# Kernel tuning notes

Measured on AMD Instinct MI355X. Metric: run time of the kernel, lower is better.

The kernel has to match this reference:

```python
import jax, jax.numpy as jnp
import numpy as np

LAMBDA = 0.2
BETA = 1.0
EPS = 1e-6


def setup_inputs() -> dict:
    key = jax.random.key(0)
    t_prime = jax.random.normal(key, (8192, 768), dtype=jnp.float32)
    return {"t_prime": t_prime}


def reference(t_prime) -> jnp.ndarray:
    vocab = t_prime.shape[0]
    # L2-normalize rows (matches F.normalize p=2, dim=1 with its 1e-12 clamp)
    norm = jnp.maximum(jnp.linalg.norm(t_prime, axis=1, keepdims=True), 1e-12)
    t_norm = t_prime / norm
    # [vocab, vocab] cosine similarity
    S = t_norm @ t_norm.T
    diag = jnp.diagonal(S)
    collapse = jnp.sum((diag - 1.0) ** 2)
    # HNS path: off-diagonal entries per row, expressed without boolean reshape.
    # neg_sims = S with diagonal removed; reweight * neg^2 = beta * neg^3 / (mean_neg + eps)
    S_off = S - jnp.diag(diag)  # zero diagonal == off-diagonal values
    mean_neg = jnp.sum(S_off, axis=1) / (vocab - 1)  # per-row mean of negatives
    row_cube = jnp.sum(S_off ** 3, axis=1)  # diagonal contributes 0
    hard_neg_loss = BETA * jnp.sum(row_cube / (mean_neg + EPS))
    return collapse + LAMBDA * hard_neg_loss
```

## Files before the change

kernel.cpp:

```cpp
#include <hip/hip_runtime.h>
#include <math.h>

#define VV 8192
#define DD 768
#define NDMAX 256

typedef __attribute__((ext_vector_type(8))) short bf16x8;
typedef __attribute__((ext_vector_type(4))) float f32x4;

__device__ inline ushort f2bf(float f) {
    uint u = __float_as_uint(f);
    uint r = (u + 0x7fffu + ((u >> 16) & 1u)) >> 16;
    return (ushort)r;
}
__device__ inline float bf2f(ushort h) { return __uint_as_float(((uint)h) << 16); }

__device__ inline void gload16(const ushort* g, ushort* l) {
    __builtin_amdgcn_global_load_lds(
        (const __attribute__((address_space(1))) void*)g,
        (__attribute__((address_space(3))) void*)l, 16, 0, 0);
}

__global__ __launch_bounds__(256) void k_normfused(const float* __restrict__ t,
                                                   float* __restrict__ norms,
                                                   ushort* __restrict__ xh,
                                                   ushort* __restrict__ xl,
                                                   double* __restrict__ gp,
                                                   float* __restrict__ rc,
                                                   int* __restrict__ dlist,
                                                   int* __restrict__ dcount) {
    const int tid = threadIdx.x;
    const int r0 = blockIdx.x * 16;
    if (tid < 16) rc[r0 + tid] = 0.f;
    if (blockIdx.x == 0) {
        dlist[tid] = -1;
        if (tid == 0) *dcount = 0;
    }
    __shared__ double wsum[2][4];
    const int lane = tid & 63, w = tid >> 6;
    double s0 = 0.0, s1 = 0.0, s2 = 0.0;
    for (int rr = 0; rr < 16; rr += 2) {
        const float* trA = t + (size_t)(r0 + rr) * DD;
        const float* trB = trA + DD;
        float a0 = trA[tid], a1 = trA[tid + 256], a2 = trA[tid + 512];
        float b0 = trB[tid], b1 = trB[tid + 256], b2 = trB[tid + 512];
        double sA = (double)a0 * a0 + (double)a1 * a1 + (double)a2 * a2;
        double sB = (double)b0 * b0 + (double)b1 * b1 + (double)b2 * b2;
#pragma unroll
        for (int o = 32; o > 0; o >>= 1) {
            sA += __shfl_down(sA, o, 64);
            sB += __shfl_down(sB, o, 64);
        }
        if (lane == 0) { wsum[0][w] = sA; wsum[1][w] = sB; }
        __syncthreads();
        float nA = fmaxf((float)sqrt(wsum[0][0] + wsum[0][1] + wsum[0][2] + wsum[0][3]), 1e-12f);
        float nB = fmaxf((float)sqrt(wsum[1][0] + wsum[1][1] + wsum[1][2] + wsum[1][3]), 1e-12f);
        __syncthreads();
        if (tid == 0) {
            norms[r0 + rr] = nA;
            norms[r0 + rr + 1] = nB;
        }
        size_t baseA = (size_t)(r0 + rr) * DD, baseB = baseA + DD;
        float xA0 = a0 / nA, xA1 = a1 / nA, xA2 = a2 / nA;
        float xB0 = b0 / nB, xB1 = b1 / nB, xB2 = b2 / nB;
        ushort h;
        h = f2bf(xA0); xh[baseA + tid] = h;       xl[baseA + tid] = f2bf(xA0 - bf2f(h));
        h = f2bf(xA1); xh[baseA + tid + 256] = h; xl[baseA + tid + 256] = f2bf(xA1 - bf2f(h));
        h = f2bf(xA2); xh[baseA + tid + 512] = h; xl[baseA + tid + 512] = f2bf(xA2 - bf2f(h));
        h = f2bf(xB0); xh[baseB + tid] = h;       xl[baseB + tid] = f2bf(xB0 - bf2f(h));
        h = f2bf(xB1); xh[baseB + tid + 256] = h; xl[baseB + tid + 256] = f2bf(xB1 - bf2f(h));
        h = f2bf(xB2); xh[baseB + tid + 512] = h; xl[baseB + tid + 512] = f2bf(xB2 - bf2f(h));
        s0 += (double)xA0; s0 += (double)xB0;
        s1 += (double)xA1; s1 += (double)xB1;
        s2 += (double)xA2; s2 += (double)xB2;
    }
    double* gb = gp + (size_t)blockIdx.x * DD;
    gb[tid] = s0;
    gb[tid + 256] = s1;
    gb[tid + 512] = s2;
}

__global__ __launch_bounds__(256) void k_colsumB(const double* __restrict__ gp,
                                                 double* __restrict__ g) {
    __shared__ double red[8][32];
    int c = threadIdx.x & 31, part = threadIdx.x >> 5;
    int col = blockIdx.x * 32 + c;
    double s = 0.0;
    for (int b = part * 64; b < part * 64 + 64; ++b)
        s += gp[(size_t)b * DD + col];
    red[part][c] = s;
    __syncthreads();
    if (part == 0) {
        double tt = 0.0;
        for (int p = 0; p < 8; ++p) tt += red[p][c];
        g[col] = tt;
    }
}

__global__ __launch_bounds__(256) void k_mean(const float* __restrict__ t,
                                              const float* __restrict__ norms,
                                              const double* __restrict__ g,
                                              double* __restrict__ mnum,
                                              double* __restrict__ dd,
                                              int* __restrict__ dlist,
                                              int* __restrict__ dcount) {
    int r = blockIdx.x * 4 + (threadIdx.x >> 6);
    int lane = threadIdx.x & 63;
    const float* tr = t + (size_t)r * DD;
    float nrm = norms[r];
    double xg = 0.0, xx = 0.0;
#pragma unroll
    for (int k = lane; k < DD; k += 64) {
        float xf = tr[k] / nrm;
        double xv = (double)xf;
        xg += xv * g[k];
        xx += xv * xv;
    }
#pragma unroll
    for (int o = 32; o > 0; o >>= 1) {
        xg += __shfl_down(xg, o, 64);
        xx += __shfl_down(xx, o, 64);
    }
    if (lane == 0) {
        double m = xg - xx;
        mnum[r] = m;
        dd[r] = xx;
        if (fabs(m / 8191.0 + 1e-6) < 1e-5) {
            int pos = atomicAdd(dcount, 1);
            if (pos < NDMAX) dlist[pos] = r;
        }
    }
}

__global__ __launch_bounds__(256, 2) void k_cube(const ushort* __restrict__ xh,
                                                 const ushort* __restrict__ xl,
                                                 const int* __restrict__ dlist,
                                                 float* __restrict__ Sb,
                                                 float* __restrict__ rc) {
    __shared__ ushort As0[4096], As1[4096], As2[4096];
    __shared__ ushort Bs0[8192], Bs1[8192], Bs2[8192];

    const int bid = blockIdx.x;
    const int tid = threadIdx.x;
    const int lane = tid & 63;
    const int wid = tid >> 6;
    const int l15 = lane & 15, li4 = lane >> 4;
    const int wm = wid >> 1, wn = wid & 1;

    const bool strip = (bid < 192);
    int bi = 0, bj = 0, seg = 0, rp = 0, cp = 0;
    if (strip) {
        seg = bid >> 6;
        int rem = bid & 63;
        rp = rem >> 5;
        cp = rem & 31;
        if (dlist[rp * 128] < 0) return;
    } else {
        int idx = bid - 192;
        int wg = (idx & 7) * 132 + (idx >> 3);
        int j = 0;
        while (wg >= 2 * j + 2) { wg -= 2 * j + 2; ++j; }
        bi = wg;
        bj = j;
    }
    const ushort* XA = strip ? ((seg == 1) ? xl : xh) : xh;
    const ushort* XB = strip ? ((seg == 2) ? xl : xh) : xh;

    int asrc[2], bsrc[4], lda_[2], ldb_[4];
#pragma unroll
    for (int j = 0; j < 2; ++j) {
        int li = tid + j * 256;
        int row = li >> 2;
        int sl = ((li & 3) ^ ((li >> 3) & 3)) * 8;
        int ar = strip ? dlist[rp * 128 + row] : (bi * 128 + row);
        if (ar < 0) ar = 0;
        asrc[j] = ar * DD + sl;
        lda_[j] = li * 8;
    }
#pragma unroll
    for (int j = 0; j < 4; ++j) {
        int li = tid + j * 256;
        int row = li >> 2;
        int sl = ((li & 3) ^ ((li >> 3) & 3)) * 8;
        int br = strip ? (cp * 256 + row) : (bj * 256 + row);
        bsrc[j] = br * DD + sl;
        ldb_[j] = li * 8;
    }

    const int swz = (li4 ^ ((l15 >> 1) & 3)) << 3;
    const int aoff = (wm * 64 + l15) * 32 + swz;
    const int boff = (wn * 128 + l15) * 32 + swz;

    f32x4 acc[4][8];
#pragma unroll
    for (int f = 0; f < 4; ++f)
#pragma unroll
        for (int n = 0; n < 8; ++n) acc[f][n] = (f32x4){0.f, 0.f, 0.f, 0.f};

#define STG(AW, BW, KT)                                  \
    do {                                                 \
        const int kq_ = (KT) * 32;                       \
        gload16(XA + asrc[0] + kq_, (AW) + lda_[0]);     \
        gload16(XA + asrc[1] + kq_, (AW) + lda_[1]);     \
        gload16(XB + bsrc[0] + kq_, (BW) + ldb_[0]);     \
        gload16(XB + bsrc[1] + kq_, (BW) + ldb_[1]);     \
        gload16(XB + bsrc[2] + kq_, (BW) + ldb_[2]);     \
        gload16(XB + bsrc[3] + kq_, (BW) + ldb_[3]);     \
    } while (0)

#define COMPUTE(AR, BR)                                                     \
    do {                                                                    \
        bf16x8 av[4], bv[8];                                                \
        _Pragma("unroll") for (int f = 0; f < 4; ++f)                       \
            av[f] = *(const bf16x8*)((AR) + aoff + f * 512);                \
        _Pragma("unroll") for (int n = 0; n < 8; ++n)                       \
            bv[n] = *(const bf16x8*)((BR) + boff + n * 512);                \
        _Pragma("unroll") for (int f = 0; f < 4; ++f)                       \
            _Pragma("unroll") for (int n = 0; n < 8; ++n)                   \
                acc[f][n] = __builtin_amdgcn_mfma_f32_16x16x32_bf16(        \
                    av[f], bv[n], acc[f][n], 0, 0, 0);                      \
    } while (0)

#define VMW6() asm volatile("s_waitcnt vmcnt(6)" ::: "memory")
#define VMW0() asm volatile("s_waitcnt vmcnt(0)" ::: "memory")
#define RBAR() asm volatile("s_barrier" ::: "memory")

    STG(As0, Bs0, 0);
    STG(As1, Bs1, 1);
    VMW6(); RBAR();

    for (int tb = 0; tb < 21; tb += 3) {
        STG(As2, Bs2, tb + 2);
        COMPUTE(As0, Bs0);
        VMW6(); RBAR();
        STG(As0, Bs0, tb + 3);
        COMPUTE(As1, Bs1);
        VMW6(); RBAR();
        STG(As1, Bs1, tb + 4);
        COMPUTE(As2, Bs2);
        VMW6(); RBAR();
    }
    STG(As2, Bs2, 23);
    COMPUTE(As0, Bs0);
    VMW6(); RBAR();
    COMPUTE(As1, Bs1);
    VMW0(); RBAR();
    COMPUTE(As2, Bs2);
#undef STG
#undef COMPUTE
#undef VMW6
#undef VMW0
#undef RBAR

    if (strip) {
#pragma unroll
        for (int f = 0; f < 4; ++f)
#pragma unroll
            for (int n = 0; n < 8; ++n)
#pragma unroll
                for (int r = 0; r < 4; ++r) {
                    int slot = seg * 256 + rp * 128 + wm * 64 + f * 16 + li4 * 4 + r;
                    int col = cp * 256 + wn * 128 + n * 16 + l15;
                    Sb[((size_t)slot << 13) + col] = acc[f][n][r];
                }
        return;
    }

    const bool dtile = ((bi >> 1) == bj);
    const int R0 = bi * 128, C0 = bj * 256;
    float rsum[4][4], csum[8];
#pragma unroll
    for (int n = 0; n < 8; ++n) csum[n] = 0.f;
#pragma unroll
    for (int f = 0; f < 4; ++f)
#pragma unroll
        for (int r = 0; r < 4; ++r) rsum[f][r] = 0.f;
#pragma unroll
    for (int f = 0; f < 4; ++f)
#pragma unroll
        for (int n = 0; n < 8; ++n)
#pragma unroll
            for (int r = 0; r < 4; ++r) {
                float s = acc[f][n][r];
                float c = s * s * s;
                int ri = R0 + wm * 64 + f * 16 + li4 * 4 + r;
                int cj = C0 + wn * 128 + n * 16 + l15;
                if (dtile && ri == cj) c = 0.f;
                rsum[f][r] += c;
                csum[n] += c;
            }
#pragma unroll
    for (int o = 1; o < 16; o <<= 1)
#pragma unroll
        for (int f = 0; f < 4; ++f)
#pragma unroll
            for (int r = 0; r < 4; ++r)
                rsum[f][r] += __shfl_xor(rsum[f][r], o, 64);
    if (l15 == 0) {
#pragma unroll
        for (int f = 0; f < 4; ++f)
#pragma unroll
            for (int r = 0; r < 4; ++r)
                atomicAdd(&rc[R0 + wm * 64 + f * 16 + li4 * 4 + r], rsum[f][r]);
    }
    if (!dtile) {
#pragma unroll
        for (int o = 16; o < 64; o <<= 1)
#pragma unroll
            for (int n = 0; n < 8; ++n) csum[n] += __shfl_xor(csum[n], o, 64);
        if (li4 == 0) {
#pragma unroll
            for (int n = 0; n < 8; ++n)
                atomicAdd(&rc[C0 + wn * 128 + n * 16 + l15], csum[n]);
        }
    }
}

__global__ __launch_bounds__(256) void k_cubefin(const float* __restrict__ Sb,
                                                 const int* __restrict__ dlist,
                                                 float* __restrict__ rc) {
    const int slot = blockIdx.x;
    const int drow = dlist[slot];
    if (drow < 0) return;
    const int tid = threadIdx.x;
    const float* s0p = Sb + ((size_t)slot << 13);
    const float* s1p = Sb + ((size_t)(256 + slot) << 13);
    const float* s2p = Sb + ((size_t)(512 + slot) << 13);
    float sum = 0.f;
    for (int c = tid; c < VV; c += 256) {
        float s0 = s0p[c];
        float sf = s0 + s1p[c] + s2p[c];
        float d = sf * sf * sf - s0 * s0 * s0;
        if (c == drow) d = 0.f;
        sum += d;
    }
    __shared__ float red[256];
    red[tid] = sum;
    __syncthreads();
    for (int o = 128; o > 0; o >>= 1) {
        if (tid < o) red[tid] += red[tid + o];
        __syncthreads();
    }
    if (tid == 0) atomicAdd(&rc[drow], red[0]);
}

__global__ __launch_bounds__(1024) void k_final(const float* __restrict__ rc,
                                                const double* __restrict__ mnum,
                                                const double* __restrict__ dd,
                                                float* __restrict__ out) {
    int tid = threadIdx.x;
    double acc = 0.0, col = 0.0;
    for (int r = tid; r < VV; r += 1024) {
        double m = mnum[r] / 8191.0 + 1e-6;
        acc += (double)rc[r] / m;
        double dm = dd[r] - 1.0;
        col += dm * dm;
    }
    __shared__ double sa[1024], sc[1024];
    sa[tid] = acc;
    sc[tid] = col;
    __syncthreads();
    for (int o = 512; o > 0; o >>= 1) {
        if (tid < o) {
            sa[tid] += sa[tid + o];
            sc[tid] += sc[tid + o];
        }
        __syncthreads();
    }
    if (tid == 0) out[0] = (float)(sc[0] + 0.2 * sa[0]);
}

extern "C" void kernel_launch(void* const* d_in, const int* in_sizes, int n_in,
                              void* d_out, int out_size, void* d_ws, size_t ws_size,
                              hipStream_t stream) {
    const float* t = (const float*)d_in[0];
    float* out = (float*)d_out;

    char* ws = (char*)d_ws;
    float* Sb = (float*)ws;
    size_t off = (size_t)VV * DD * sizeof(float);
    ushort* xh = (ushort*)(ws + off); off += (size_t)VV * DD * sizeof(ushort);
    ushort* xl = (ushort*)(ws + off); off += (size_t)VV * DD * sizeof(ushort);
    double* g = (double*)(ws + off);  off += DD * sizeof(double);
    double* mnum = (double*)(ws + off); off += VV * sizeof(double);
    double* dd = (double*)(ws + off);  off += VV * sizeof(double);
    float* rc = (float*)(ws + off);    off += VV * sizeof(float);
    int* dlist = (int*)(ws + off);     off += NDMAX * sizeof(int);
    int* dcount = (int*)(ws + off);    off += sizeof(int) + 60;
    float* norms = (float*)(ws + off); off += VV * sizeof(float);
    double* gp = (double*)(ws + off);  off += (size_t)512 * DD * sizeof(double);

    k_normfused<<<512, 256, 0, stream>>>(t, norms, xh, xl, gp, rc, dlist, dcount);
    k_colsumB<<<24, 256, 0, stream>>>(gp, g);
    k_mean<<<VV / 4, 256, 0, stream>>>(t, norms, g, mnum, dd, dlist, dcount);
    k_cube<<<1248, 256, 0, stream>>>(xh, xl, dlist, Sb, rc);
    k_cubefin<<<NDMAX, 256, 0, stream>>>(Sb, dlist, rc);
    k_final<<<1, 1024, 0, stream>>>(rc, mnum, dd, out);
}
```

Before: 121.1 us.

## Split tail triangle tiles into half-width blocks to balance final wave

The last 224 triangle tiles of the symmetric S=XX^T cube-sum kernel are now each split into two 128x128 half tiles, handled by extra blocks (1472 instead of 1248). The main loop moves into a templated helper so half blocks load and multiply only half the B columns, with their own epilogue for row and column cube sums. The aim is to shrink the tail wave imbalance across CUs. The cost is extra A-tile reloads and more atomics for those tiles.

```diff
diff --git a/kernel.cpp b/kernel.cpp
--- a/kernel.cpp
+++ b/kernel.cpp
@@ -132,6 +132,81 @@
     }
 }
 
+template <int NLB>
+__device__ __forceinline__ void cube_loop(
+    const ushort* __restrict__ XA, const ushort* __restrict__ XB,
+    int asrc0, int asrc1, int bsrc0, int bsrc1, int bsrc2, int bsrc3,
+    int lda0, int lda1, int ldb0, int ldb1, int ldb2, int ldb3,
+    int aoff, int boff,
+    ushort* As0, ushort* As1, ushort* As2,
+    ushort* Bs0, ushort* Bs1, ushort* Bs2,
+    f32x4 (&acc)[4][8]) {
+    constexpr int NB = 2 * NLB;
+
+#define STG(AW, BW, KT)                                                  \
+    do {                                                                 \
+        const int kq_ = (KT) * 32;                                       \
+        gload16(XA + asrc0 + kq_, (AW) + lda0);                          \
+        gload16(XA + asrc1 + kq_, (AW) + lda1);                          \
+        gload16(XB + bsrc0 + kq_, (BW) + ldb0);                          \
+        gload16(XB + bsrc1 + kq_, (BW) + ldb1);                          \
+        if constexpr (NLB == 4) {                                        \
+            gload16(XB + bsrc2 + kq_, (BW) + ldb2);                      \
+            gload16(XB + bsrc3 + kq_, (BW) + ldb3);                      \
+        }                                                                \
+    } while (0)
+
+#define COMPUTE(AR, BR)                                                     \
+    do {                                                                    \
+        bf16x8 av[4], bv[NB];                                               \
+        _Pragma("unroll") for (int f = 0; f < 4; ++f)                       \
+            av[f] = *(const bf16x8*)((AR) + aoff + f * 512);                \
+        _Pragma("unroll") for (int n = 0; n < NB; ++n)                      \
+            bv[n] = *(const bf16x8*)((BR) + boff + n * 512);                \
+        _Pragma("unroll") for (int f = 0; f < 4; ++f)                       \
+            _Pragma("unroll") for (int n = 0; n < NB; ++n)                  \
+                acc[f][n] = __builtin_amdgcn_mfma_f32_16x16x32_bf16(        \
+                    av[f], bv[n], acc[f][n], 0, 0, 0);                      \
+    } while (0)
+
+#define VMWP()                                                           \
+    do {                                                                 \
+        if constexpr (NLB == 4)                                          \
+            asm volatile("s_waitcnt vmcnt(6)" ::: "memory");              \
+        else                                                             \
+            asm volatile("s_waitcnt vmcnt(4)" ::: "memory");              \
+    } while (0)
+#define VMW0() asm volatile("s_waitcnt vmcnt(0)" ::: "memory")
+#define RBAR() asm volatile("s_barrier" ::: "memory")
+
+    STG(As0, Bs0, 0);
+    STG(As1, Bs1, 1);
+    VMWP(); RBAR();
+
+    for (int tb = 0; tb < 21; tb += 3) {
+        STG(As2, Bs2, tb + 2);
+        COMPUTE(As0, Bs0);
+        VMWP(); RBAR();
+        STG(As0, Bs0, tb + 3);
+        COMPUTE(As1, Bs1);
+        VMWP(); RBAR();
+        STG(As1, Bs1, tb + 4);
+        COMPUTE(As2, Bs2);
+        VMWP(); RBAR();
+    }
+    STG(As2, Bs2, 23);
+    COMPUTE(As0, Bs0);
+    VMWP(); RBAR();
+    COMPUTE(As1, Bs1);
+    VMW0(); RBAR();
+    COMPUTE(As2, Bs2);
+#undef STG
+#undef COMPUTE
+#undef VMWP
+#undef VMW0
+#undef RBAR
+}
+
 __global__ __launch_bounds__(256, 2) void k_cube(const ushort* __restrict__ xh,
                                                  const ushort* __restrict__ xl,
                                                  const int* __restrict__ dlist,
@@ -148,7 +223,8 @@
     const int wm = wid >> 1, wn = wid & 1;
 
     const bool strip = (bid < 192);
-    int bi = 0, bj = 0, seg = 0, rp = 0, cp = 0;
+    const bool half = (bid >= 1024);
+    int bi = 0, bj = 0, seg = 0, rp = 0, cp = 0, hh = 0;
     if (strip) {
         seg = bid >> 6;
         int rem = bid & 63;
@@ -156,8 +232,16 @@
         cp = rem & 31;
         if (dlist[rp * 128] < 0) return;
     } else {
-        int idx = bid - 192;
-        int wg = (idx & 7) * 132 + (idx >> 3);
+        int wg;
+        if (!half) {
+            int idx = bid - 192;
+            wg = (idx & 7) * 132 + (idx >> 3);
+        } else {
+            int hx = bid - 1024;
+            int q = hx >> 1;
+            hh = hx & 1;
+            wg = (q & 7) * 132 + 104 + (q >> 3);
+        }
         int j = 0;
         while (wg >= 2 * j + 2) { wg -= 2 * j + 2; ++j; }
         bi = wg;
@@ -166,7 +250,7 @@
     const ushort* XA = strip ? ((seg == 1) ? xl : xh) : xh;
     const ushort* XB = strip ? ((seg == 2) ? xl : xh) : xh;
 
-    int asrc[2], bsrc[4], lda_[2], ldb_[4];
+    int asrc[2], bsrc[4] = {0, 0, 0, 0}, lda_[2], ldb_[4] = {0, 0, 0, 0};
 #pragma unroll
     for (int j = 0; j < 2; ++j) {
         int li = tid + j * 256;
@@ -177,19 +261,20 @@
         asrc[j] = ar * DD + sl;
         lda_[j] = li * 8;
     }
-#pragma unroll
-    for (int j = 0; j < 4; ++j) {
+    const int nbl = half ? 2 : 4;
+    for (int j = 0; j < nbl; ++j) {
         int li = tid + j * 256;
         int row = li >> 2;
         int sl = ((li & 3) ^ ((li >> 3) & 3)) * 8;
-        int br = strip ? (cp * 256 + row) : (bj * 256 + row);
+        int br = strip ? (cp * 256 + row)
+                       : (bj * 256 + (half ? hh * 128 : 0) + row);
         bsrc[j] = br * DD + sl;
         ldb_[j] = li * 8;
     }
 
     const int swz = (li4 ^ ((l15 >> 1) & 3)) << 3;
     const int aoff = (wm * 64 + l15) * 32 + swz;
-    const int boff = (wn * 128 + l15) * 32 + swz;
+    const int boff = ((wn * (half ? 64 : 128)) + l15) * 32 + swz;
 
     f32x4 acc[4][8];
 #pragma unroll
@@ -197,60 +282,64 @@
 #pragma unroll
         for (int n = 0; n < 8; ++n) acc[f][n] = (f32x4){0.f, 0.f, 0.f, 0.f};
 
-#define STG(AW, BW, KT)                                  \
-    do {                                                 \
-        const int kq_ = (KT) * 32;                       \
-        gload16(XA + asrc[0] + kq_, (AW) + lda_[0]);     \
-        gload16(XA + asrc[1] + kq_, (AW) + lda_[1]);     \
-        gload16(XB + bsrc[0] + kq_, (BW) + ldb_[0]);     \
-        gload16(XB + bsrc[1] + kq_, (BW) + ldb_[1]);     \
-        gload16(XB + bsrc[2] + kq_, (BW) + ldb_[2]);     \
-        gload16(XB + bsrc[3] + kq_, (BW) + ldb_[3]);     \
-    } while (0)
-
-#define COMPUTE(AR, BR)                                                     \
-    do {                                                                    \
-        bf16x8 av[4], bv[8];                                                \
-        _Pragma("unroll") for (int f = 0; f < 4; ++f)                       \
-            av[f] = *(const bf16x8*)((AR) + aoff + f * 512);                \
-        _Pragma("unroll") for (int n = 0; n < 8; ++n)                       \
-            bv[n] = *(const bf16x8*)((BR) + boff + n * 512);                \
-        _Pragma("unroll") for (int f = 0; f < 4; ++f)                       \
-            _Pragma("unroll") for (int n = 0; n < 8; ++n)                   \
-                acc[f][n] = __builtin_amdgcn_mfma_f32_16x16x32_bf16(        \
-                    av[f], bv[n], acc[f][n], 0, 0, 0);                      \
-    } while (0)
-
-#define VMW6() asm volatile("s_waitcnt vmcnt(6)" ::: "memory")
-#define VMW0() asm volatile("s_waitcnt vmcnt(0)" ::: "memory")
-#define RBAR() asm volatile("s_barrier" ::: "memory")
-
-    STG(As0, Bs0, 0);
-    STG(As1, Bs1, 1);
-    VMW6(); RBAR();
-
-    for (int tb = 0; tb < 21; tb += 3) {
-        STG(As2, Bs2, tb + 2);
-        COMPUTE(As0, Bs0);
-        VMW6(); RBAR();
-        STG(As0, Bs0, tb + 3);
-        COMPUTE(As1, Bs1);
-        VMW6(); RBAR();
-        STG(As1, Bs1, tb + 4);
-        COMPUTE(As2, Bs2);
-        VMW6(); RBAR();
-    }
-    STG(As2, Bs2, 23);
-    COMPUTE(As0, Bs0);
-    VMW6(); RBAR();
-    COMPUTE(As1, Bs1);
-    VMW0(); RBAR();
-    COMPUTE(As2, Bs2);
-#undef STG
-#undef COMPUTE
-#undef VMW6
-#undef VMW0
-#undef RBAR
+    if (half) {
+        cube_loop<2>(XA, XB, asrc[0], asrc[1], bsrc[0], bsrc[1], bsrc[2], bsrc[3],
+                     lda_[0], lda_[1], ldb_[0], ldb_[1], ldb_[2], ldb_[3],
+                     aoff, boff, As0, As1, As2, Bs0, Bs1, Bs2, acc);
+        const bool dtile = ((bi >> 1) == bj);
+        const int R0 = bi * 128, C0 = bj * 256 + hh * 128;
+        float rsum[4][4], csum[4];
+#pragma unroll
+        for (int n = 0; n < 4; ++n) csum[n] = 0.f;
+#pragma unroll
+        for (int f = 0; f < 4; ++f)
+#pragma unroll
+            for (int r = 0; r < 4; ++r) rsum[f][r] = 0.f;
+#pragma unroll
+        for (int f = 0; f < 4; ++f)
+#pragma unroll
+            for (int n = 0; n < 4; ++n)
+#pragma unroll
+                for (int r = 0; r < 4; ++r) {
+                    float s = acc[f][n][r];
+                    float c = s * s * s;
+                    int ri = R0 + wm * 64 + f * 16 + li4 * 4 + r;
+                    int cj = C0 + wn * 64 + n * 16 + l15;
+                    if (dtile && ri == cj) c = 0.f;
+                    rsum[f][r] += c;
+                    csum[n] += c;
+                }
+#pragma unroll
+        for (int o = 1; o < 16; o <<= 1)
+#pragma unroll
+            for (int f = 0; f < 4; ++f)
+#pragma unroll
+                for (int r = 0; r < 4; ++r)
+                    rsum[f][r] += __shfl_xor(rsum[f][r], o, 64);
+        if (l15 == 0) {
+#pragma unroll
+            for (int f = 0; f < 4; ++f)
+#pragma unroll
+                for (int r = 0; r < 4; ++r)
+                    atomicAdd(&rc[R0 + wm * 64 + f * 16 + li4 * 4 + r], rsum[f][r]);
+        }
+        if (!dtile) {
+#pragma unroll
+            for (int o = 16; o < 64; o <<= 1)
+#pragma unroll
+                for (int n = 0; n < 4; ++n) csum[n] += __shfl_xor(csum[n], o, 64);
+            if (li4 == 0) {
+#pragma unroll
+                for (int n = 0; n < 4; ++n)
+                    atomicAdd(&rc[C0 + wn * 64 + n * 16 + l15], csum[n]);
+            }
+        }
+        return;
+    }
+
+    cube_loop<4>(XA, XB, asrc[0], asrc[1], bsrc[0], bsrc[1], bsrc[2], bsrc[3],
+                 lda_[0], lda_[1], ldb_[0], ldb_[1], ldb_[2], ldb_[3],
+                 aoff, boff, As0, As1, As2, Bs0, Bs1, Bs2, acc);
 
     if (strip) {
 #pragma unroll
@@ -393,7 +482,7 @@
     k_normfused<<<512, 256, 0, stream>>>(t, norms, xh, xl, gp, rc, dlist, dcount);
     k_colsumB<<<24, 256, 0, stream>>>(gp, g);
     k_mean<<<VV / 4, 256, 0, stream>>>(t, norms, g, mnum, dd, dlist, dcount);
-    k_cube<<<1248, 256, 0, stream>>>(xh, xl, dlist, Sb, rc);
+    k_cube<<<1472, 256, 0, stream>>>(xh, xl, dlist, Sb, rc);
     k_cubefin<<<NDMAX, 256, 0, stream>>>(Sb, dlist, rc);
     k_final<<<1, 1024, 0, stream>>>(rc, mnum, dd, out);
 }
```

After: 129.4 us. 6.9% more time.
